# Kernel optimization log

Measured on AMD Instinct MI355X. Metric: run time of the kernel, lower is better.

The kernel has to match this reference:

```python
import jax, jax.numpy as jnp
import numpy as np

N_USERS = 20000
N_ITEMS = 30000
N = N_USERS + N_ITEMS          # total nodes
D = 64                          # embedding_dim
EXTRA = 1152                    # 768 metadata + 384 review
E = 500000                      # full-graph edges
NC = 100                        # clusters
HEADS = 2                       # per-layer GATConv heads
CG_HEADS = 4                    # GlobalGATOverClusters hard-codes heads=4
L = 2                           # num_layers
ED = 2                          # edge_dim


def _gat(x, ei, ea, lin, a_src, a_dst, lin_e, a_edge, bias, heads, nnodes):
    """PyG GATConv: add self loops (edge_attr fill='mean'), concat=False -> head mean."""
    C = a_src.shape[-1]
    loop = jnp.arange(nnodes)
    src = jnp.concatenate([ei[0], loop])
    dst = jnp.concatenate([ei[1], loop])
    ea_full = jnp.concatenate([ea, jnp.broadcast_to(ea.mean(0), (nnodes, ea.shape[1]))], 0)
    xh = (x @ lin).reshape(nnodes, heads, C)            # [N,H,C]
    asrc = (xh * a_src).sum(-1)                         # [N,H]
    adst = (xh * a_dst).sum(-1)
    eh = (ea_full @ lin_e).reshape(-1, heads, C)        # [Etot,H,C]
    ae = (eh * a_edge).sum(-1)                          # [Etot,H]
    al = jax.nn.leaky_relu(asrc[src] + adst[dst] + ae, 0.2)
    amax = jax.ops.segment_max(al, dst, num_segments=nnodes)
    ex = jnp.exp(al - amax[dst])
    s = jax.ops.segment_sum(ex, dst, num_segments=nnodes)
    w = ex / (s[dst] + 1e-16)
    out = jax.ops.segment_sum(xh[src] * w[..., None], dst, num_segments=nnodes)
    return out.mean(1) + bias


def _graph_norm(x, weight, bias, mean_scale, eps=1e-5):
    mean = x.mean(0)
    out = x - mean_scale * mean
    var = (out * out).mean(0)
    return weight * out * jax.lax.rsqrt(var + eps) + bias


def _forward(product_extra_features, user_emb, item_emb, fus_w1, fus_b1, fus_w2, fus_b2,
             full_edge_attr, gcn_w, gcn_b,
             cg_lin, cg_att_src, cg_att_dst, cg_lin_edge, cg_att_edge, cg_bias, cluster_edge_attr,
             gat_lin, gat_att_src, gat_att_dst, gat_lin_edge, gat_att_edge, gat_bias,
             gn_weight, gn_bias, gn_mean_scale,
             full_edge_index, cluster_assignment, cluster_edge_index):
    # fusion MLP on item side (dropout is identity at inference)
    h = jnp.maximum(jnp.concatenate([item_emb, product_extra_features], -1) @ fus_w1 + fus_b1, 0.0)
    enriched_items = h @ fus_w2 + fus_b2
    X = jnp.concatenate([user_emb, enriched_items], 0)  # [N, D]

    # per-cluster GCN == one GCN over intra-cluster edges + self loops;
    # nodes in clusters with zero intra edges keep original features
    ei0, ei1 = full_edge_index[0], full_edge_index[1]
    intra = cluster_assignment[ei0] == cluster_assignment[ei1]
    loop = jnp.arange(N)
    row = jnp.concatenate([ei0, loop])
    col = jnp.concatenate([ei1, loop])
    ew = jnp.concatenate([intra.astype(X.dtype), jnp.ones((N,), X.dtype)])
    deg = jax.ops.segment_sum(ew, col, num_segments=N)
    dinv = jnp.where(deg > 0, jax.lax.rsqrt(deg), 0.0)
    norm = dinv[row] * ew * dinv[col]
    xw = X @ gcn_w
    gcn_out = jax.ops.segment_sum(xw[row] * norm[:, None], col, num_segments=N) + gcn_b
    cl_has_edge = jax.ops.segment_sum(intra.astype(jnp.int32), cluster_assignment[ei0], num_segments=NC) > 0
    Xc = jnp.where(cl_has_edge[cluster_assignment][:, None], gcn_out, X)

    # mean pool per cluster
    cnt = jax.ops.segment_sum(jnp.ones((N,), X.dtype), cluster_assignment, num_segments=NC)
    pooled = jax.ops.segment_sum(Xc, cluster_assignment, num_segments=NC) / jnp.maximum(cnt, 1.0)[:, None]

    # global GAT over clusters (inter-cluster multigraph, precomputed)
    cl_upd = _gat(pooled, cluster_edge_index, cluster_edge_attr,
                  cg_lin, cg_att_src, cg_att_dst, cg_lin_edge, cg_att_edge, cg_bias, CG_HEADS, NC)
    Xcomb = Xc + cl_upd[cluster_assignment]

    # full-graph GAT stack with GraphNorm + residual ELU (dropout identity)
    for i in range(L):
        Xin = Xcomb
        g = _gat(Xcomb, full_edge_index, full_edge_attr,
                 gat_lin[i], gat_att_src[i], gat_att_dst[i],
                 gat_lin_edge[i], gat_att_edge[i], gat_bias[i], HEADS, N)
        g = _graph_norm(g, gn_weight[i], gn_bias[i], gn_mean_scale[i])
        Xcomb = jax.nn.elu(g + Xin)

    return Xcomb[:N_USERS], Xcomb[N_USERS:]


def setup_inputs() -> dict:
    rng = np.random.default_rng(0)
    fei = rng.integers(0, N, size=(2, E)).astype(np.int32)
    ca = rng.integers(0, NC, size=(N,)).astype(np.int32)
    fea = rng.random((E, ED)).astype(np.float32)
    # build_cluster_graph: one cluster edge per inter-cluster full edge
    cu, cv = ca[fei[0]], ca[fei[1]]
    m = cu != cv
    cei = np.stack([cu[m], cv[m]]).astype(np.int32)
    cea = fea[m]

    key = jax.random.key(0)
    ks = jax.random.split(key, 24)
    nrm = lambda k, shp, s=0.05: jax.random.normal(k, shp, dtype=jnp.float32) * s
    return {
        'product_extra_features': jax.random.normal(ks[0], (N_ITEMS, EXTRA), dtype=jnp.float32),
        'user_emb': nrm(ks[1], (N_USERS, D), 1.0),
        'item_emb': nrm(ks[2], (N_ITEMS, D), 1.0),
        'fus_w1': nrm(ks[3], (D + EXTRA, 2 * D)),
        'fus_b1': jnp.zeros((2 * D,), jnp.float32),
        'fus_w2': nrm(ks[4], (2 * D, D)),
        'fus_b2': jnp.zeros((D,), jnp.float32),
        'full_edge_attr': jnp.asarray(fea),
        'gcn_w': nrm(ks[5], (D, D)),
        'gcn_b': jnp.zeros((D,), jnp.float32),
        'cg_lin': nrm(ks[6], (D, CG_HEADS * D)),
        'cg_att_src': nrm(ks[7], (CG_HEADS, D)),
        'cg_att_dst': nrm(ks[8], (CG_HEADS, D)),
        'cg_lin_edge': nrm(ks[9], (ED, CG_HEADS * D)),
        'cg_att_edge': nrm(ks[10], (CG_HEADS, D)),
        'cg_bias': jnp.zeros((D,), jnp.float32),
        'cluster_edge_attr': jnp.asarray(cea),
        'gat_lin': nrm(ks[11], (L, D, HEADS * D)),
        'gat_att_src': nrm(ks[12], (L, HEADS, D)),
        'gat_att_dst': nrm(ks[13], (L, HEADS, D)),
        'gat_lin_edge': nrm(ks[14], (L, ED, HEADS * D)),
        'gat_att_edge': nrm(ks[15], (L, HEADS, D)),
        'gat_bias': jnp.zeros((L, D), jnp.float32),
        'gn_weight': jnp.ones((L, D), jnp.float32),
        'gn_bias': jnp.zeros((L, D), jnp.float32),
        'gn_mean_scale': jnp.ones((L, D), jnp.float32),
        'full_edge_index': jnp.asarray(fei),
        'cluster_assignment': jnp.asarray(ca),
        'cluster_edge_index': jnp.asarray(cei),
    }


def reference(product_extra_features, user_emb, item_emb, fus_w1, fus_b1, fus_w2, fus_b2,
              full_edge_attr, gcn_w, gcn_b,
              cg_lin, cg_att_src, cg_att_dst, cg_lin_edge, cg_att_edge, cg_bias, cluster_edge_attr,
              gat_lin, gat_att_src, gat_att_dst, gat_lin_edge, gat_att_edge, gat_bias,
              gn_weight, gn_bias, gn_mean_scale,
              full_edge_index, cluster_assignment, cluster_edge_index):
    return _forward(product_extra_features, user_emb, item_emb, fus_w1, fus_b1, fus_w2, fus_b2,
                    full_edge_attr, gcn_w, gcn_b,
                    cg_lin, cg_att_src, cg_att_dst, cg_lin_edge, cg_att_edge, cg_bias, cluster_edge_attr,
                    gat_lin, gat_att_src, gat_att_dst, gat_lin_edge, gat_att_edge, gat_bias,
                    gn_weight, gn_bias, gn_mean_scale,
                    full_edge_index, cluster_assignment, cluster_edge_index)
```

## Files before the change

kernel.cpp:

```cpp
#include <hip/hip_runtime.h>
#include <hip/hip_bf16.h>

#define N_USERS 20000
#define N_ITEMS 30000
#define NTOT    50000
#define DIM     64
#define EXTRA_D 1152
#define E_EDGES 500000
#define NC      100
#define KTOT    1216
#define KSTEPS  38
#define PPART   16

#define B_COPY 1250
#define B_W1   608
#define B_W2   32
#define B_CC   64
#define B_FEI  1954
#define B_CEI  256
#define PREP_GRID (B_COPY+B_W1+B_W2+B_CC+B_FEI+B_CEI)

#define FUS_BLKS ((N_ITEMS+127)/128)
#define SCAN1_BLKS ((NTOT+1023)/1024)
#define SC3_BLKS ((NTOT+255)/256)
#define FILL_BLKS ((E_EDGES+255)/256)
#define DEG_BLKS ((NTOT+3)/4)

typedef __attribute__((ext_vector_type(8))) short short8;
typedef __attribute__((ext_vector_type(4))) float v4f;

__device__ __forceinline__ float wred_sum(float v){
#pragma unroll
  for(int o=32;o;o>>=1) v += __shfl_xor(v,o,64);
  return v;
}
__device__ __forceinline__ int wred_sumi(int v){
#pragma unroll
  for(int o=32;o;o>>=1) v += __shfl_xor(v,o,64);
  return v;
}
__device__ __forceinline__ float lrelu(float x){ return x>0.f? x : 0.2f*x; }
__device__ __forceinline__ short f2bf(float f){
  unsigned u=__float_as_uint(f);
  unsigned r=(u + 0x7FFFu + ((u>>16)&1u))>>16;
  return (short)r;
}
__device__ __forceinline__ unsigned pack_bf2(float x, float y){
  return (unsigned)(unsigned short)f2bf(x) | ((unsigned)(unsigned short)f2bf(y)<<16);
}

__global__ __launch_bounds__(256) void prep_all_kernel(
    const float* __restrict__ u, float* __restrict__ X,
    const float* __restrict__ w1, short* __restrict__ w1t,
    const float* __restrict__ w2, short* __restrict__ w2t,
    const int* __restrict__ ca, int* __restrict__ ccnt,
    const int* __restrict__ fei, const float* __restrict__ fea,
    int* __restrict__ cnt_dst, int* __restrict__ clflag, int* __restrict__ degI,
    float2* __restrict__ partA,
    const int* __restrict__ cei, const float* __restrict__ cea, int Ec,
    int* __restrict__ ccnt_dst, float2* __restrict__ partB)
{
  __shared__ int hist[NC];
  __shared__ float2 w4[4];
  const int b=blockIdx.x, t=threadIdx.x;
  const int lane=t&63, wv=t>>6;
  if(b < B_COPY){
    int i = b*256+t;
    ((float4*)X)[i] = ((const float4*)u)[i];
  } else if(b < B_COPY+B_W1){
    int i = (b-B_COPY)*256+t;
    int row = i>>7, n = i&127;
    int s = row>>5, kk = row&31;
    w1t[s*4096 + n*32 + kk] = f2bf(w1[i]);
  } else if(b < B_COPY+B_W1+B_W2){
    int i = (b-B_COPY-B_W1)*256+t;
    int n = i>>6, c = i&63;
    w2t[c*128 + n] = f2bf(w2[i]);
  } else if(b < B_COPY+B_W1+B_W2+B_CC){
    int bb = b-(B_COPY+B_W1+B_W2);
    for(int i=t;i<NC;i+=256) hist[i]=0;
    __syncthreads();
    for(int n=bb*256+t; n<NTOT; n+=B_CC*256) atomicAdd(&hist[ca[n]],1);
    __syncthreads();
    for(int i=t;i<NC;i+=256) if(hist[i]) atomicAdd(&ccnt[i],hist[i]);
  } else if(b < B_COPY+B_W1+B_W2+B_CC+B_FEI){
    int bb = b-(B_COPY+B_W1+B_W2+B_CC);
    int e = bb*256+t;
    float a0=0.f,a1=0.f;
    if(e<E_EDGES){
      int s=fei[e], d=fei[E_EDGES+e];
      atomicAdd(&cnt_dst[d],1);
      int cs=ca[s];
      if(cs==ca[d]){ clflag[cs]=1; atomicAdd(&degI[d],1); }
      float2 v=*(const float2*)(fea+2*e);
      a0=v.x; a1=v.y;
    }
    a0=wred_sum(a0); a1=wred_sum(a1);
    if(lane==0) w4[wv]=make_float2(a0,a1);
    __syncthreads();
    if(t==0){ float2 r=w4[0]; for(int i=1;i<4;i++){r.x+=w4[i].x; r.y+=w4[i].y;} partA[bb]=r; }
  } else {
    int bb = b-(B_COPY+B_W1+B_W2+B_CC+B_FEI);
    for(int i=t;i<NC;i+=256) hist[i]=0;
    __syncthreads();
    float a0=0.f,a1=0.f;
    for(int e=bb*256+t; e<Ec; e+=B_CEI*256){
      atomicAdd(&hist[cei[Ec+e]],1);
      float2 v=*(const float2*)(cea+2*e);
      a0+=v.x; a1+=v.y;
    }
    a0=wred_sum(a0); a1=wred_sum(a1);
    if(lane==0) w4[wv]=make_float2(a0,a1);
    __syncthreads();
    if(t==0){ float2 r=w4[0]; for(int i=1;i<4;i++){r.x+=w4[i].x; r.y+=w4[i].y;} partB[bb]=r; }
    for(int i=t;i<NC;i+=256) if(hist[i]) atomicAdd(&ccnt_dst[i],hist[i]);
  }
}

__global__ __launch_bounds__(256) void fus_scan_kernel(
    const float* __restrict__ item, const float* __restrict__ extra,
    const short* __restrict__ w1t, const float* __restrict__ b1,
    const short* __restrict__ w2t, const float* __restrict__ b2,
    float* __restrict__ X,
    const float2* __restrict__ partA, const float2* __restrict__ partB, int Ec,
    const float* __restrict__ cg_le, const float* __restrict__ cg_ae,
    const float* __restrict__ gat_le, const float* __restrict__ gat_ae,
    float* __restrict__ coefs,
    const int* __restrict__ cnt_dst, int* __restrict__ incl, int* __restrict__ bsum)
{
  __shared__ short As[128*40];
  __shared__ short Bs[128*40];
  __shared__ short Hs[128*136];
  __shared__ int ssc[256];
  const int tid = threadIdx.x;
  const int b = blockIdx.x;
  if(b < FUS_BLKS){
    const int blk = b;
    const int w = tid>>6, lane = tid&63, quad = lane>>4, l16 = lane&15;
    const int mw = w&1, nw = w>>1;

    v4f acc[4][4];
#pragma unroll
    for(int a=0;a<4;a++)
#pragma unroll
      for(int c=0;c<4;c++) acc[a][c] = (v4f){0.f,0.f,0.f,0.f};

    const int arow = tid>>3;
    const int aoff = (tid&7)*4;
    for(int s=0;s<KSTEPS;s++){
      const int k0 = s*32;
#pragma unroll
      for(int it=0;it<4;it++){
        int r = arow + it*32;
        int col = k0 + aoff;
        int gr = blk*128 + r; if(gr >= N_ITEMS) gr = N_ITEMS-1;
        float4 v = (col < DIM) ? *(const float4*)(item + (size_t)gr*DIM + col)
                               : *(const float4*)(extra + (size_t)gr*EXTRA_D + (col-DIM));
        short4 bv; bv.x=f2bf(v.x); bv.y=f2bf(v.y); bv.z=f2bf(v.z); bv.w=f2bf(v.w);
        *(short4*)&As[r*40 + aoff] = bv;
      }
#pragma unroll
      for(int it=0;it<2;it++){
        int idx = tid + it*256;
        int4 v = *(const int4*)(w1t + (size_t)s*4096 + idx*8);
        int n = idx>>2, kk = (idx&3)*8;
        *(int4*)&Bs[n*40 + kk] = v;
      }
      __syncthreads();
      short8 af[4], bf_[4];
#pragma unroll
      for(int i=0;i<4;i++){
        int m = mw*64 + i*16 + l16;
        af[i]  = *(const short8*)&As[m*40 + quad*8];
        int n = nw*64 + i*16 + l16;
        bf_[i] = *(const short8*)&Bs[n*40 + quad*8];
      }
#pragma unroll
      for(int mi=0;mi<4;mi++)
#pragma unroll
        for(int ni=0;ni<4;ni++)
          acc[mi][ni] = __builtin_amdgcn_mfma_f32_16x16x32_bf16(af[mi], bf_[ni], acc[mi][ni], 0,0,0);
      __syncthreads();
    }

#pragma unroll
    for(int ni=0;ni<4;ni++){
      int n = nw*64 + ni*16 + l16;
      float bias = b1[n];
#pragma unroll
      for(int mi=0;mi<4;mi++){
        int mbase = mw*64 + mi*16 + quad*4;
#pragma unroll
        for(int r=0;r<4;r++){
          float hv = fmaxf(acc[mi][ni][r] + bias, 0.f);
          Hs[(mbase+r)*136 + n] = f2bf(hv);
        }
      }
    }
    __syncthreads();

    v4f acc2[2][4];
#pragma unroll
    for(int a=0;a<2;a++)
#pragma unroll
      for(int c=0;c<4;c++) acc2[a][c] = (v4f){0.f,0.f,0.f,0.f};
#pragma unroll
    for(int ks=0;ks<4;ks++){
      short8 ha[2];
#pragma unroll
      for(int mi=0;mi<2;mi++){
        int m = w*32 + mi*16 + l16;
        ha[mi] = *(const short8*)&Hs[m*136 + ks*32 + quad*8];
      }
#pragma unroll
      for(int ni=0;ni<4;ni++){
        int c = ni*16 + l16;
        short8 wb = *(const short8*)(w2t + c*128 + ks*32 + quad*8);
#pragma unroll
        for(int mi=0;mi<2;mi++)
          acc2[mi][ni] = __builtin_amdgcn_mfma_f32_16x16x32_bf16(ha[mi], wb, acc2[mi][ni], 0,0,0);
      }
    }
#pragma unroll
    for(int ni=0;ni<4;ni++){
      int c = ni*16 + l16;
      float b2v = b2[c];
#pragma unroll
      for(int mi=0;mi<2;mi++){
        int mbase = w*32 + mi*16 + quad*4;
#pragma unroll
        for(int r=0;r<4;r++){
          int row = blk*128 + mbase + r;
          if(row < N_ITEMS) X[(size_t)(N_USERS+row)*64 + c] = acc2[mi][ni][r] + b2v;
        }
      }
    }
  } else if(b == FUS_BLKS){
    int lane=tid&63; int wv=tid>>6;
    {
      int hh=wv;
      float v0 = cg_le[hh*64+lane]*cg_ae[hh*64+lane];
      float v1 = cg_le[256 + hh*64+lane]*cg_ae[hh*64+lane];
      v0=wred_sum(v0); v1=wred_sum(v1);
      if(lane==0){ coefs[8+hh]=v0; coefs[12+hh]=v1; }
    }
    {
      int l=wv>>1, hh=wv&1;
      float v0 = gat_le[l*256 + hh*64+lane]     * gat_ae[l*128+hh*64+lane];
      float v1 = gat_le[l*256 + 128 + hh*64+lane]* gat_ae[l*128+hh*64+lane];
      v0=wred_sum(v0); v1=wred_sum(v1);
      if(lane==0){ coefs[16+l*2+hh]=v0; coefs[20+l*2+hh]=v1; }
    }
    __syncthreads();
    if(wv==0){
      float sx=0.f, sy=0.f;
      for(int i=lane;i<B_FEI;i+=64){ float2 v=partA[i]; sx+=v.x; sy+=v.y; }
      sx=wred_sum(sx); sy=wred_sum(sy);
      if(lane==0){ coefs[4]=sx/(float)E_EDGES; coefs[5]=sy/(float)E_EDGES; }
    }
    if(wv==1){
      float sx=0.f, sy=0.f;
      for(int i=lane;i<B_CEI;i+=64){ float2 v=partB[i]; sx+=v.x; sy+=v.y; }
      sx=wred_sum(sx); sy=wred_sum(sy);
      if(lane==0){ coefs[6]=sx/(float)Ec; coefs[7]=sy/(float)Ec; }
    }
  } else {
    int sb = b-FUS_BLKS-1;
    int base = sb*1024 + tid*4;
    int a0=(base  <NTOT)?cnt_dst[base  ]+1:0;
    int a1=(base+1<NTOT)?cnt_dst[base+1]+1:0;
    int a2=(base+2<NTOT)?cnt_dst[base+2]+1:0;
    int a3=(base+3<NTOT)?cnt_dst[base+3]+1:0;
    int l1=a0+a1, l2=l1+a2, l3=l2+a3;
    ssc[tid]=l3; __syncthreads();
    for(int off=1;off<256;off<<=1){
      int v=(tid>=off)?ssc[tid-off]:0; __syncthreads();
      ssc[tid]+=v; __syncthreads();
    }
    int prev = tid? ssc[tid-1]:0;
    if(base  <NTOT) incl[base  ]=prev+a0;
    if(base+1<NTOT) incl[base+1]=prev+l1;
    if(base+2<NTOT) incl[base+2]=prev+l2;
    if(base+3<NTOT) incl[base+3]=prev+l3;
    if(tid==255) bsum[sb]=ssc[255];
  }
}

__global__ __launch_bounds__(256) void mid_kernel(
    const int* __restrict__ incl, const int* __restrict__ cnt,
    const int* __restrict__ bsum, int* __restrict__ offs, int* __restrict__ fillptr,
    const float* __restrict__ coefs, int2* __restrict__ slot2,
    const int* __restrict__ degI, float* __restrict__ dinv,
    const int* __restrict__ ccnt_dst, int* __restrict__ coffs, int* __restrict__ cfillp,
    const float* __restrict__ X, const float* __restrict__ gw, float* __restrict__ xw)
{
  __shared__ float Wl[64*64];
  __shared__ float rowb[4][64];
  __shared__ int sprev;
  const int b=blockIdx.x, t=threadIdx.x;
  if(b < SC3_BLKS){
    int blk10 = b>>2;
    if(t<64){
      int v = (t<blk10)? bsum[t] : 0;
      v = wred_sumi(v);
      if(t==0) sprev=v;
    }
    __syncthreads();
    unsigned pk = pack_bf2(coefs[4], coefs[5]);
    int i = b*256+t;
    if(i<NTOT){
      int c=cnt[i];
      int start = sprev + incl[i] - (c+1);
      offs[i]=start; fillptr[i]=start;
      slot2[start+c]=make_int2(i,(int)pk);
      dinv[i]=rsqrtf((float)(degI[i]+1));
    }
    if(i==0) offs[NTOT]=E_EDGES+NTOT;
  } else if(b == SC3_BLKS){
    if(t<64){
      int lane=t;
      int v0 = (2*lane<NC)? ccnt_dst[2*lane]:0;
      int v1 = (2*lane+1<NC)? ccnt_dst[2*lane+1]:0;
      int pair=v0+v1;
      int sc=pair;
#pragma unroll
      for(int o=1;o<64;o<<=1){ int t2=__shfl_up(sc,o,64); if(lane>=o) sc+=t2; }
      int excl = sc - pair;
      if(2*lane<NC){ coffs[2*lane]=excl; cfillp[2*lane]=excl; }
      if(2*lane+1<NC){ coffs[2*lane+1]=excl+v0; cfillp[2*lane+1]=excl+v0; }
      if(lane==63) coffs[NC]=sc;
    }
  } else {
    int bb=b-SC3_BLKS-1;
    const int lane=t&63, wv=t>>6;
    for(int i=t;i<4096;i+=256) Wl[i]=gw[i];
    __syncthreads();
    for(int r=bb*4+wv; r<NTOT; r+=1024*4){
      rowb[wv][lane]=X[(size_t)r*64+lane];
      float acc=0.f;
#pragma unroll 8
      for(int k=0;k<64;k++) acc+=rowb[wv][k]*Wl[k*64+lane];
      xw[(size_t)r*64+lane]=acc;
    }
  }
}

__global__ __launch_bounds__(256) void fill_kernel(
    const int* __restrict__ fei, const float* __restrict__ fea,
    int* __restrict__ fillptr, int2* __restrict__ slot2,
    const int* __restrict__ cei, const float* __restrict__ cea, int Ec,
    int* __restrict__ cfillp, int* __restrict__ cslot_src, float2* __restrict__ cslot_ea)
{
  __shared__ int hist[NC];
  __shared__ int base[NC];
  const int b=blockIdx.x, t=threadIdx.x;
  if(b<FILL_BLKS){
    int e=b*256+t;
    if(e<E_EDGES){
      int dst=fei[E_EDGES+e], src=fei[e];
      int pos=atomicAdd(&fillptr[dst],1);
      float2 v=*(const float2*)(fea+2*e);
      slot2[pos]=make_int2(src,(int)pack_bf2(v.x,v.y));
    }
  } else {
    int bb=b-FILL_BLKS;
    const int chunk=(Ec+127)/128;
    const int beg=bb*chunk;
    const int end=min(beg+chunk,Ec);
    for(int i=t;i<NC;i+=256) hist[i]=0;
    __syncthreads();
    for(int e=beg+t;e<end;e+=256) atomicAdd(&hist[cei[Ec+e]],1);
    __syncthreads();
    for(int i=t;i<NC;i+=256){
      int h=hist[i];
      base[i] = h ? atomicAdd(&cfillp[i],h) : 0;
      hist[i]=0;
    }
    __syncthreads();
    for(int e=beg+t;e<end;e+=256){
      int d=cei[Ec+e];
      int pos = base[d] + atomicAdd(&hist[d],1);
      cslot_src[pos]=cei[e];
      cslot_ea[pos]=make_float2(cea[2*e],cea[2*e+1]);
    }
  }
}

__global__ __launch_bounds__(256) void gcn_agg_kernel(const float* __restrict__ X,
    const float* __restrict__ xw, const float* __restrict__ gcn_b,
    const int* __restrict__ offs, const int2* __restrict__ slot2, const int* __restrict__ ca,
    const float* __restrict__ dinv, const int* __restrict__ flag,
    float* __restrict__ Xc, float* __restrict__ psum){
  __shared__ float2 stg[4][64];
  int lane=threadIdx.x&63, wv=threadIdx.x>>6;
  int n=blockIdx.x*4+wv; if(n>=NTOT) return;
  int beg=offs[n], end=offs[n+1], myca=ca[n];
  float acc=0.f;
  for(int c0=beg;c0<end;c0+=64){
    int j=c0+lane;
    float coef=0.f; int s=0;
    if(j<end){
      s=slot2[j].x;
      if(ca[s]==myca) coef=dinv[s];
    }
    stg[wv][lane]=make_float2(__int_as_float(s),coef);
    unsigned long long bal=__ballot(coef!=0.f);
    while(bal){
      int k=__builtin_ctzll(bal); bal&=bal-1;
      float2 sc=stg[wv][k];
      acc += sc.y * xw[(size_t)__float_as_int(sc.x)*64+lane];
    }
  }
  float gout = dinv[n]*acc + gcn_b[lane];
  float xc = flag[myca] ? gout : X[(size_t)n*64+lane];
  Xc[(size_t)n*64+lane]=xc;
  atomicAdd(&psum[(size_t)(blockIdx.x&(PPART-1))*NC*64 + myca*64+lane], xc);
}

__global__ __launch_bounds__(256) void cluster_prep_kernel(const float* __restrict__ psum,
    const int* __restrict__ ccnt, const float* __restrict__ cg_lin,
    const float* __restrict__ as_, const float* __restrict__ ad_,
    float* __restrict__ xh_c, float* __restrict__ asrc_c, float* __restrict__ adst_c){
  __shared__ float prow[64];
  const int c=blockIdx.x, t=threadIdx.x;
  if(t<64){
    float a=0.f;
#pragma unroll
    for(int p=0;p<PPART;p++) a += psum[(size_t)p*NC*64 + c*64 + t];
    prow[t]=a/fmaxf((float)ccnt[c],1.f);
  }
  __syncthreads();
  float acc=0.f;
#pragma unroll 8
  for(int k=0;k<64;k++) acc += prow[k]*cg_lin[k*256+t];
  xh_c[c*256+t]=acc;
  int lane=t&63, hh=t>>6;
  float s=wred_sum(acc*as_[hh*64+lane]);
  float d=wred_sum(acc*ad_[hh*64+lane]);
  if(lane==0){ asrc_c[c*4+hh]=s; adst_c[c*4+hh]=d; }
}
__global__ __launch_bounds__(256) void cluster_agg_kernel(
    const int* __restrict__ coffs, const int* __restrict__ cslot_src, const float2* __restrict__ cslot_ea,
    const float* __restrict__ asrc_c, const float* __restrict__ adst_c, const float* __restrict__ coefs,
    const float* __restrict__ xh_c, const float* __restrict__ cg_bias, float* __restrict__ cl_upd)
{
  __shared__ float sas[NC*4];
  __shared__ float sW[NC*4];
  __shared__ float ssum[4];
  __shared__ float red[4][64];
  const int c=blockIdx.x, t=threadIdx.x;
  for(int i=t;i<NC*4;i+=256){ sas[i]=asrc_c[i]; sW[i]=0.f; }
  __syncthreads();
  float ad[4], A0[4], A1[4];
#pragma unroll
  for(int h=0;h<4;h++){ ad[h]=adst_c[c*4+h]; A0[h]=coefs[8+h]; A1[h]=coefs[12+h]; }
  const int beg=coffs[c], end=coffs[c+1];
  for(int j=beg+t;j<end;j+=256){
    int s=cslot_src[j]; float2 e=cslot_ea[j];
#pragma unroll
    for(int h=0;h<4;h++){
      float al=lrelu(sas[s*4+h]+ad[h]+e.x*A0[h]+e.y*A1[h]);
      atomicAdd(&sW[s*4+h], __expf(al));
    }
  }
  if(t<4){
    float al=lrelu(sas[c*4+t]+ad[t]+coefs[6]*A0[t]+coefs[7]*A1[t]);
    atomicAdd(&sW[c*4+t], __expf(al));
  }
  __syncthreads();
  const int h=t>>6, lane=t&63;
  float p=0.f;
  if(lane<NC)    p += sW[lane*4+h];
  if(lane+64<NC) p += sW[(lane+64)*4+h];
  p=wred_sum(p);
  if(lane==0) ssum[h]=p+1e-16f;
  __syncthreads();
  float inv=1.f/ssum[h];
  float acc=0.f;
  for(int s=0;s<NC;s++) acc += sW[s*4+h]*xh_c[s*256+h*64+lane];
  red[h][lane]=acc*inv;
  __syncthreads();
  if(t<64) cl_upd[c*64+t]=0.25f*(red[0][t]+red[1][t]+red[2][t]+red[3][t])+cg_bias[t];
}

__global__ __launch_bounds__(256) void gat_xh0_kernel(const float* __restrict__ Xc,
    const float* __restrict__ cl_upd, const int* __restrict__ ca,
    const float* __restrict__ lin, const float* __restrict__ att_s, const float* __restrict__ att_d,
    float2* __restrict__ xh2, float* __restrict__ asrc, float* __restrict__ adst,
    float* __restrict__ Xa){
  __shared__ __align__(16) float Wl[64*128];
  __shared__ float rowb[4][64];
  int t=threadIdx.x;
  for(int i=t;i<8192;i+=256) Wl[i]=lin[i];
  __syncthreads();
  int lane=t&63, wv=t>>6;
  float as0=att_s[lane], as1=att_s[64+lane], ad0=att_d[lane], ad1=att_d[64+lane];
  for(int r=blockIdx.x*4+wv; r<NTOT; r+=gridDim.x*4){
    float xv = Xc[(size_t)r*64+lane] + cl_upd[ca[r]*64+lane];
    Xa[(size_t)r*64+lane]=xv;
    rowb[wv][lane]=xv;
    float x0=0.f,x1=0.f;
#pragma unroll 8
    for(int k=0;k<64;k++){ float q=rowb[wv][k]; x0+=q*Wl[k*128+lane]; x1+=q*Wl[k*128+64+lane]; }
    xh2[(size_t)r*64+lane]=make_float2(x0,x1);
    float p0=wred_sum(x0*as0);
    float p1=wred_sum(x1*as1);
    float q0=wred_sum(x0*ad0);
    float q1=wred_sum(x1*ad1);
    if(lane==0){ asrc[2*r]=p0; asrc[2*r+1]=p1; adst[2*r]=q0; adst[2*r+1]=q1; }
  }
}
__global__ __launch_bounds__(256) void gat_xh1_kernel(const float* __restrict__ g,
    const float* __restrict__ Xres, const float* __restrict__ stats,
    const float* __restrict__ gnw, const float* __restrict__ gnb, const float* __restrict__ gnms,
    const float* __restrict__ lin, const float* __restrict__ att_s, const float* __restrict__ att_d,
    float2* __restrict__ xh2, float* __restrict__ asrc, float* __restrict__ adst,
    float* __restrict__ Xb){
  __shared__ __align__(16) float Wl[64*128];
  __shared__ float rowb[4][64];
  int t=threadIdx.x;
  for(int i=t;i<8192;i+=256) Wl[i]=lin[i];
  __syncthreads();
  int lane=t&63, wv=t>>6;
  const float invN = 1.f/(float)NTOT;
  float m=stats[lane]*invN;
  float mm=gnms[lane]*m;
  float gwv=rsqrtf(stats[64+lane]*invN - 2.f*mm*m + mm*mm + 1e-5f)*gnw[lane];
  float gbv=gnb[lane];
  float as0=att_s[lane], as1=att_s[64+lane], ad0=att_d[lane], ad1=att_d[64+lane];
  for(int r=blockIdx.x*4+wv; r<NTOT; r+=gridDim.x*4){
    float z=(g[(size_t)r*64+lane]-mm)*gwv+gbv + Xres[(size_t)r*64+lane];
    float xv = z>0.f? z : __expf(z)-1.f;
    Xb[(size_t)r*64+lane]=xv;
    rowb[wv][lane]=xv;
    float x0=0.f,x1=0.f;
#pragma unroll 8
    for(int k=0;k<64;k++){ float q=rowb[wv][k]; x0+=q*Wl[k*128+lane]; x1+=q*Wl[k*128+64+lane]; }
    xh2[(size_t)r*64+lane]=make_float2(x0,x1);
    float p0=wred_sum(x0*as0);
    float p1=wred_sum(x1*as1);
    float q0=wred_sum(x0*ad0);
    float q1=wred_sum(x1*ad1);
    if(lane==0){ asrc[2*r]=p0; asrc[2*r+1]=p1; adst[2*r]=q0; adst[2*r+1]=q1; }
  }
}

__global__ __launch_bounds__(256) void gat_agg_kernel(const float2* __restrict__ xh2,
    const float2* __restrict__ asrc, const float2* __restrict__ adst,
    const int* __restrict__ offs, const int2* __restrict__ slot2,
    const float* __restrict__ coefs, int layer, const float* __restrict__ bias,
    float* __restrict__ g){
  __shared__ float4 stg[4][64];
  int lane=threadIdx.x&63, wv=threadIdx.x>>6;
  int n=blockIdx.x*4+wv; if(n>=NTOT) return;
  float A00=coefs[16+layer*2+0], A01=coefs[16+layer*2+1];
  float A10=coefs[20+layer*2+0], A11=coefs[20+layer*2+1];
  int beg=offs[n], end=offs[n+1];
  float2 adn=adst[n];
  float s0=0.f,s1=0.f,acc0=0.f,acc1=0.f;
  for(int c0=beg;c0<end;c0+=64){
    int j=c0+lane;
    float ex0=0.f,ex1=0.f; int s=0;
    if(j<end){
      int2 sl=slot2[j];
      s=sl.x;
      unsigned p=(unsigned)sl.y;
      float e0=__uint_as_float(p<<16);
      float e1=__uint_as_float(p&0xffff0000u);
      float2 a=asrc[s];
      ex0=__expf(lrelu(a.x+adn.x+e0*A00+e1*A10));
      ex1=__expf(lrelu(a.y+adn.y+e0*A01+e1*A11));
    }
    s0+=ex0; s1+=ex1;
    stg[wv][lane]=make_float4(__int_as_float(s),ex0,ex1,0.f);
    int cnt=min(64,end-c0);
    int k=0;
    for(; k+4<=cnt; k+=4){
      float4 w0=stg[wv][k], w1=stg[wv][k+1], w2=stg[wv][k+2], w3=stg[wv][k+3];
      float2 x0=xh2[(size_t)__float_as_int(w0.x)*64+lane];
      float2 x1=xh2[(size_t)__float_as_int(w1.x)*64+lane];
      float2 x2=xh2[(size_t)__float_as_int(w2.x)*64+lane];
      float2 x3=xh2[(size_t)__float_as_int(w3.x)*64+lane];
      acc0 += w0.y*x0.x + w1.y*x1.x + w2.y*x2.x + w3.y*x3.x;
      acc1 += w0.z*x0.y + w1.z*x1.y + w2.z*x2.y + w3.z*x3.y;
    }
    for(; k<cnt; k++){
      float4 ws=stg[wv][k];
      float2 xv=xh2[(size_t)__float_as_int(ws.x)*64+lane];
      acc0 += ws.y*xv.x;
      acc1 += ws.z*xv.y;
    }
  }
  s0=wred_sum(s0); s1=wred_sum(s1);
  g[(size_t)n*64+lane]=0.5f*(acc0/(s0+1e-16f)+acc1/(s1+1e-16f))+bias[lane];
}
__global__ __launch_bounds__(256) void stats_kernel(const float* __restrict__ g,
    float* __restrict__ stats){
  __shared__ float s1[64], s2[64];
  int t=threadIdx.x;
  if(t<64){s1[t]=0.f;s2[t]=0.f;}
  __syncthreads();
  float a0=0.f,a1=0.f,a2=0.f,a3=0.f,b0=0.f,b1=0.f,b2=0.f,b3=0.f;
  int i0=blockIdx.x*256+t;
  for(int i=i0;i<NTOT*16;i+=gridDim.x*256){
    float4 v=((const float4*)g)[i];
    a0+=v.x;a1+=v.y;a2+=v.z;a3+=v.w;
    b0+=v.x*v.x;b1+=v.y*v.y;b2+=v.z*v.z;b3+=v.w*v.w;
  }
  int d0=(i0&15)*4;
  atomicAdd(&s1[d0],a0); atomicAdd(&s1[d0+1],a1); atomicAdd(&s1[d0+2],a2); atomicAdd(&s1[d0+3],a3);
  atomicAdd(&s2[d0],b0); atomicAdd(&s2[d0+1],b1); atomicAdd(&s2[d0+2],b2); atomicAdd(&s2[d0+3],b3);
  __syncthreads();
  if(t<64) atomicAdd(&stats[t],s1[t]);
  else if(t<128) atomicAdd(&stats[t],s2[t-64]);
}
__global__ __launch_bounds__(256) void gnorm_elu_kernel(const float* __restrict__ g,
    const float* __restrict__ Xin, const float* __restrict__ stats,
    const float* __restrict__ gw, const float* __restrict__ gb, const float* __restrict__ gms,
    float* __restrict__ outp){
  const float invN = 1.f/(float)NTOT;
  int i0=blockIdx.x*256+threadIdx.x;
  int d0=(i0&15)*4;
  float mmv[4],gwv[4],gbv[4];
#pragma unroll
  for(int j=0;j<4;j++){
    int d=d0+j;
    float m=stats[d]*invN;
    float mm=gms[d]*m;
    mmv[j]=mm;
    gwv[j]=rsqrtf(stats[64+d]*invN-2.f*mm*m+mm*mm+1e-5f)*gw[d];
    gbv[j]=gb[d];
  }
  for(int i=i0;i<NTOT*16;i+=gridDim.x*256){
    float4 gv=((const float4*)g)[i];
    float4 xv=((const float4*)Xin)[i];
    float4 o; float z;
    z=(gv.x-mmv[0])*gwv[0]+gbv[0]+xv.x; o.x = z>0.f? z : __expf(z)-1.f;
    z=(gv.y-mmv[1])*gwv[1]+gbv[1]+xv.y; o.y = z>0.f? z : __expf(z)-1.f;
    z=(gv.z-mmv[2])*gwv[2]+gbv[2]+xv.z; o.z = z>0.f? z : __expf(z)-1.f;
    z=(gv.w-mmv[3])*gwv[3]+gbv[3]+xv.w; o.w = z>0.f? z : __expf(z)-1.f;
    ((float4*)outp)[i]=o;
  }
}

extern "C" void kernel_launch(void* const* d_in, const int* in_sizes, int n_in,
                              void* d_out, int out_size, void* d_ws, size_t ws_size,
                              hipStream_t stream)
{
  const float* extra = (const float*)d_in[0];
  const float* user  = (const float*)d_in[1];
  const float* item  = (const float*)d_in[2];
  const float* fw1 = (const float*)d_in[3];
  const float* fb1 = (const float*)d_in[4];
  const float* fw2 = (const float*)d_in[5];
  const float* fb2 = (const float*)d_in[6];
  const float* fea = (const float*)d_in[7];
  const float* gcn_w = (const float*)d_in[8];
  const float* gcn_b = (const float*)d_in[9];
  const float* cg_lin = (const float*)d_in[10];
  const float* cg_as = (const float*)d_in[11];
  const float* cg_ad = (const float*)d_in[12];
  const float* cg_le = (const float*)d_in[13];
  const float* cg_ae = (const float*)d_in[14];
  const float* cg_bias = (const float*)d_in[15];
  const float* cea = (const float*)d_in[16];
  const float* gat_lin = (const float*)d_in[17];
  const float* gat_as = (const float*)d_in[18];
  const float* gat_ad = (const float*)d_in[19];
  const float* gat_le = (const float*)d_in[20];
  const float* gat_ae = (const float*)d_in[21];
  const float* gat_bias = (const float*)d_in[22];
  const float* gn_w = (const float*)d_in[23];
  const float* gn_b = (const float*)d_in[24];
  const float* gn_ms = (const float*)d_in[25];
  const int* fei = (const int*)d_in[26];
  const int* ca  = (const int*)d_in[27];
  const int* cei = (const int*)d_in[28];
  const int Ec = in_sizes[16]/2;
  float* outp = (float*)d_out;

  char* w = (char*)d_ws;
  auto alloc=[&](size_t b)->char*{ char* p=w; w += (b+255)&~(size_t)255; return p; };

  char* z0 = w;
  int* cnt_dst = (int*)alloc((size_t)NTOT*4);
  int* degI = (int*)alloc((size_t)NTOT*4);
  int* clflag = (int*)alloc(NC*4);
  int* ccnt = (int*)alloc(NC*4);
  int* ccnt_dst = (int*)alloc(NC*4);
  float* psum = (float*)alloc((size_t)PPART*NC*64*4);
  float* stats0 = (float*)alloc(128*4);
  float* stats1 = (float*)alloc(128*4);
  size_t zbytes = (size_t)(w - z0);

  float2* partA = (float2*)alloc(2048*8);
  float2* partB = (float2*)alloc(256*8);
  float* coefs = (float*)alloc(32*4);
  int* offs = (int*)alloc((size_t)(NTOT+1)*4);
  int* incl = (int*)alloc((size_t)NTOT*4);
  int* bsum = (int*)alloc(64*4);
  int* fillptr = (int*)alloc((size_t)NTOT*4);
  int2* slot2 = (int2*)alloc((size_t)(E_EDGES+NTOT)*8);
  int* coffs = (int*)alloc((size_t)(NC+1)*4);
  int* cfillp = (int*)alloc((size_t)NC*4);
  int* cslot_src = (int*)alloc((size_t)E_EDGES*4);
  float2* cslot_ea = (float2*)alloc((size_t)E_EDGES*8);
  float* dinv = (float*)alloc((size_t)NTOT*4);
  float* xh_c = (float*)alloc(NC*256*4);
  float* asrc_c = (float*)alloc(NC*4*4);
  float* adst_c = (float*)alloc(NC*4*4);
  float* cl_upd = (float*)alloc(NC*64*4);
  float* asrc = (float*)alloc((size_t)NTOT*2*4);
  float* adst = (float*)alloc((size_t)NTOT*2*4);
  short* w1t = (short*)alloc((size_t)KSTEPS*4096*2);
  short* w2t = (short*)alloc((size_t)64*128*2);
  float* bufA = (float*)alloc((size_t)NTOT*64*4);
  float* bufB = (float*)alloc((size_t)NTOT*64*4);
  float* bufC = (float*)alloc((size_t)NTOT*64*4);
  float* bufD = (float*)alloc((size_t)NTOT*64*4);
  float* bufE = (float*)alloc((size_t)NTOT*128*4);

  float* X  = bufA; float* g  = bufA;
  float* Xc = bufB;
  float* xw = bufC; float* Xb = bufC;
  float* Xa = bufD;
  float2* xh2 = (float2*)bufE;

  hipMemsetAsync(z0, 0, zbytes, stream);

  prep_all_kernel<<<PREP_GRID,256,0,stream>>>(user, X, fw1, w1t, fw2, w2t, ca, ccnt,
                                              fei, fea, cnt_dst, clflag, degI, partA,
                                              cei, cea, Ec, ccnt_dst, partB);
  fus_scan_kernel<<<FUS_BLKS+1+SCAN1_BLKS,256,0,stream>>>(item, extra, w1t, fb1, w2t, fb2, X,
                                              partA, partB, Ec, cg_le, cg_ae, gat_le, gat_ae, coefs,
                                              cnt_dst, incl, bsum);
  mid_kernel<<<SC3_BLKS+1+1024,256,0,stream>>>(incl, cnt_dst, bsum, offs, fillptr, coefs, slot2,
                                              degI, dinv, ccnt_dst, coffs, cfillp,
                                              X, gcn_w, xw);
  fill_kernel<<<FILL_BLKS+128,256,0,stream>>>(fei, fea, fillptr, slot2,
                                              cei, cea, Ec, cfillp, cslot_src, cslot_ea);

  gcn_agg_kernel<<<DEG_BLKS,256,0,stream>>>(X, xw, gcn_b, offs, slot2, ca, dinv, clflag, Xc, psum);
  cluster_prep_kernel<<<NC,256,0,stream>>>(psum, ccnt, cg_lin, cg_as, cg_ad, xh_c, asrc_c, adst_c);
  cluster_agg_kernel<<<NC,256,0,stream>>>(coffs, cslot_src, cslot_ea, asrc_c, adst_c, coefs,
                                          xh_c, cg_bias, cl_upd);

  gat_xh0_kernel<<<1024,256,0,stream>>>(Xc, cl_upd, ca, gat_lin, gat_as, gat_ad,
                                        xh2, asrc, adst, Xa);
  gat_agg_kernel<<<DEG_BLKS,256,0,stream>>>(xh2, (const float2*)asrc, (const float2*)adst,
                                            offs, slot2, coefs, 0, gat_bias, g);
  stats_kernel<<<128,256,0,stream>>>(g, stats0);
  gat_xh1_kernel<<<1024,256,0,stream>>>(g, Xa, stats0, gn_w, gn_b, gn_ms,
                                        gat_lin+64*128, gat_as+128, gat_ad+128,
                                        xh2, asrc, adst, Xb);
  gat_agg_kernel<<<DEG_BLKS,256,0,stream>>>(xh2, (const float2*)asrc, (const float2*)adst,
                                            offs, slot2, coefs, 1, gat_bias+64, g);
  stats_kernel<<<128,256,0,stream>>>(g, stats1);
  gnorm_elu_kernel<<<512,256,0,stream>>>(g, Xb, stats1, gn_w+64, gn_b+64, gn_ms+64, outp);
}
```

Before: 671.6 us.

## Fuse stats into GAT aggregation, merge cluster kernels, rebalance prep work

Fuses the column-sum and sum-of-squares GraphNorm statistics into the GAT aggregation kernel, which removes two stats kernels and a re-read of g. The two cluster kernels are merged into one, using reassociated algebra (attention projections through cg_lin, then aggregating pooled features before the linear map) so the xh_c intermediate is dropped. The user-embedding copy and cluster-count histogram move from the prep kernel into the fusion/scan launch to balance work across kernels. In exchange, there are per-block shared atomics in the hot aggregation kernel and more global atomics on the stats arrays, and each cluster block recomputes all cluster source scores.

After: 1.225 ms. 82.4% more time.

```diff
diff --git a/kernel.cpp b/kernel.cpp
--- a/kernel.cpp
+++ b/kernel.cpp
@@ -12,16 +12,18 @@
 #define KSTEPS  38
 #define PPART   16
 
-#define B_COPY 1250
+#define B_FEI  1954
 #define B_W1   608
 #define B_W2   32
-#define B_CC   64
-#define B_FEI  1954
 #define B_CEI  256
-#define PREP_GRID (B_COPY+B_W1+B_W2+B_CC+B_FEI+B_CEI)
+#define PREP_GRID (B_FEI+B_W1+B_W2+B_CEI)
 
 #define FUS_BLKS ((N_ITEMS+127)/128)
 #define SCAN1_BLKS ((NTOT+1023)/1024)
+#define B_COPY 1250
+#define B_CC   64
+#define FUS_GRID (FUS_BLKS+SCAN1_BLKS+1+B_COPY+B_CC)
+
 #define SC3_BLKS ((NTOT+255)/256)
 #define FILL_BLKS ((E_EDGES+255)/256)
 #define DEG_BLKS ((NTOT+3)/4)
@@ -49,11 +51,10 @@
   return (unsigned)(unsigned short)f2bf(x) | ((unsigned)(unsigned short)f2bf(y)<<16);
 }
 
-__global__ __launch_bounds__(256) void prep_all_kernel(
-    const float* __restrict__ u, float* __restrict__ X,
+__global__ __launch_bounds__(256) void prep_edges_kernel(
     const float* __restrict__ w1, short* __restrict__ w1t,
     const float* __restrict__ w2, short* __restrict__ w2t,
-    const int* __restrict__ ca, int* __restrict__ ccnt,
+    const int* __restrict__ ca,
     const int* __restrict__ fei, const float* __restrict__ fea,
     int* __restrict__ cnt_dst, int* __restrict__ clflag, int* __restrict__ degI,
     float2* __restrict__ partA,
@@ -64,28 +65,8 @@
   __shared__ float2 w4[4];
   const int b=blockIdx.x, t=threadIdx.x;
   const int lane=t&63, wv=t>>6;
-  if(b < B_COPY){
-    int i = b*256+t;
-    ((float4*)X)[i] = ((const float4*)u)[i];
-  } else if(b < B_COPY+B_W1){
-    int i = (b-B_COPY)*256+t;
-    int row = i>>7, n = i&127;
-    int s = row>>5, kk = row&31;
-    w1t[s*4096 + n*32 + kk] = f2bf(w1[i]);
-  } else if(b < B_COPY+B_W1+B_W2){
-    int i = (b-B_COPY-B_W1)*256+t;
-    int n = i>>6, c = i&63;
-    w2t[c*128 + n] = f2bf(w2[i]);
-  } else if(b < B_COPY+B_W1+B_W2+B_CC){
-    int bb = b-(B_COPY+B_W1+B_W2);
-    for(int i=t;i<NC;i+=256) hist[i]=0;
-    __syncthreads();
-    for(int n=bb*256+t; n<NTOT; n+=B_CC*256) atomicAdd(&hist[ca[n]],1);
-    __syncthreads();
-    for(int i=t;i<NC;i+=256) if(hist[i]) atomicAdd(&ccnt[i],hist[i]);
-  } else if(b < B_COPY+B_W1+B_W2+B_CC+B_FEI){
-    int bb = b-(B_COPY+B_W1+B_W2+B_CC);
-    int e = bb*256+t;
+  if(b < B_FEI){
+    int e = b*256+t;
     float a0=0.f,a1=0.f;
     if(e<E_EDGES){
       int s=fei[e], d=fei[E_EDGES+e];
@@ -98,9 +79,18 @@
     a0=wred_sum(a0); a1=wred_sum(a1);
     if(lane==0) w4[wv]=make_float2(a0,a1);
     __syncthreads();
-    if(t==0){ float2 r=w4[0]; for(int i=1;i<4;i++){r.x+=w4[i].x; r.y+=w4[i].y;} partA[bb]=r; }
+    if(t==0){ float2 r=w4[0]; for(int i=1;i<4;i++){r.x+=w4[i].x; r.y+=w4[i].y;} partA[b]=r; }
+  } else if(b < B_FEI+B_W1){
+    int i = (b-B_FEI)*256+t;
+    int row = i>>7, n = i&127;
+    int s = row>>5, kk = row&31;
+    w1t[s*4096 + n*32 + kk] = f2bf(w1[i]);
+  } else if(b < B_FEI+B_W1+B_W2){
+    int i = (b-B_FEI-B_W1)*256+t;
+    int n = i>>6, c = i&63;
+    w2t[c*128 + n] = f2bf(w2[i]);
   } else {
-    int bb = b-(B_COPY+B_W1+B_W2+B_CC+B_FEI);
+    int bb = b-(B_FEI+B_W1+B_W2);
     for(int i=t;i<NC;i+=256) hist[i]=0;
     __syncthreads();
     float a0=0.f,a1=0.f;
@@ -126,7 +116,8 @@
     const float* __restrict__ cg_le, const float* __restrict__ cg_ae,
     const float* __restrict__ gat_le, const float* __restrict__ gat_ae,
     float* __restrict__ coefs,
-    const int* __restrict__ cnt_dst, int* __restrict__ incl, int* __restrict__ bsum)
+    const int* __restrict__ cnt_dst, int* __restrict__ incl, int* __restrict__ bsum,
+    const float* __restrict__ u, const int* __restrict__ ca, int* __restrict__ ccnt)
 {
   __shared__ short As[128*40];
   __shared__ short Bs[128*40];
@@ -235,37 +226,8 @@
         }
       }
     }
-  } else if(b == FUS_BLKS){
-    int lane=tid&63; int wv=tid>>6;
-    {
-      int hh=wv;
-      float v0 = cg_le[hh*64+lane]*cg_ae[hh*64+lane];
-      float v1 = cg_le[256 + hh*64+lane]*cg_ae[hh*64+lane];
-      v0=wred_sum(v0); v1=wred_sum(v1);
-      if(lane==0){ coefs[8+hh]=v0; coefs[12+hh]=v1; }
-    }
-    {
-      int l=wv>>1, hh=wv&1;
-      float v0 = gat_le[l*256 + hh*64+lane]     * gat_ae[l*128+hh*64+lane];
-      float v1 = gat_le[l*256 + 128 + hh*64+lane]* gat_ae[l*128+hh*64+lane];
-      v0=wred_sum(v0); v1=wred_sum(v1);
-      if(lane==0){ coefs[16+l*2+hh]=v0; coefs[20+l*2+hh]=v1; }
-    }
-    __syncthreads();
-    if(wv==0){
-      float sx=0.f, sy=0.f;
-      for(int i=lane;i<B_FEI;i+=64){ float2 v=partA[i]; sx+=v.x; sy+=v.y; }
-      sx=wred_sum(sx); sy=wred_sum(sy);
-      if(lane==0){ coefs[4]=sx/(float)E_EDGES; coefs[5]=sy/(float)E_EDGES; }
-    }
-    if(wv==1){
-      float sx=0.f, sy=0.f;
-      for(int i=lane;i<B_CEI;i+=64){ float2 v=partB[i]; sx+=v.x; sy+=v.y; }
-      sx=wred_sum(sx); sy=wred_sum(sy);
-      if(lane==0){ coefs[6]=sx/(float)Ec; coefs[7]=sy/(float)Ec; }
-    }
-  } else {
-    int sb = b-FUS_BLKS-1;
+  } else if(b < FUS_BLKS+SCAN1_BLKS){
+    int sb = b-FUS_BLKS;
     int base = sb*1024 + tid*4;
     int a0=(base  <NTOT)?cnt_dst[base  ]+1:0;
     int a1=(base+1<NTOT)?cnt_dst[base+1]+1:0;
@@ -283,6 +245,46 @@
     if(base+2<NTOT) incl[base+2]=prev+l2;
     if(base+3<NTOT) incl[base+3]=prev+l3;
     if(tid==255) bsum[sb]=ssc[255];
+  } else if(b == FUS_BLKS+SCAN1_BLKS){
+    int lane=tid&63; int wv=tid>>6;
+    {
+      int hh=wv;
+      float v0 = cg_le[hh*64+lane]*cg_ae[hh*64+lane];
+      float v1 = cg_le[256 + hh*64+lane]*cg_ae[hh*64+lane];
+      v0=wred_sum(v0); v1=wred_sum(v1);
+      if(lane==0){ coefs[8+hh]=v0; coefs[12+hh]=v1; }
+    }
+    {
+      int l=wv>>1, hh=wv&1;
+      float v0 = gat_le[l*256 + hh*64+lane]     * gat_ae[l*128+hh*64+lane];
+      float v1 = gat_le[l*256 + 128 + hh*64+lane]* gat_ae[l*128+hh*64+lane];
+      v0=wred_sum(v0); v1=wred_sum(v1);
+      if(lane==0){ coefs[16+l*2+hh]=v0; coefs[20+l*2+hh]=v1; }
+    }
+    __syncthreads();
+    if(wv==0){
+      float sx=0.f, sy=0.f;
+      for(int i=lane;i<B_FEI;i+=64){ float2 v=partA[i]; sx+=v.x; sy+=v.y; }
+      sx=wred_sum(sx); sy=wred_sum(sy);
+      if(lane==0){ coefs[4]=sx/(float)E_EDGES; coefs[5]=sy/(float)E_EDGES; }
+    }
+    if(wv==1){
+      float sx=0.f, sy=0.f;
+      for(int i=lane;i<B_CEI;i+=64){ float2 v=partB[i]; sx+=v.x; sy+=v.y; }
+      sx=wred_sum(sx); sy=wred_sum(sy);
+      if(lane==0){ coefs[6]=sx/(float)Ec; coefs[7]=sy/(float)Ec; }
+    }
+  } else if(b < FUS_BLKS+SCAN1_BLKS+1+B_COPY){
+    int i = (b-FUS_BLKS-SCAN1_BLKS-1)*256+tid;
+    ((float4*)X)[i] = ((const float4*)u)[i];
+  } else {
+    __shared__ int hist2[NC];
+    int bb = b-(FUS_BLKS+SCAN1_BLKS+1+B_COPY);
+    for(int i=tid;i<NC;i+=256) hist2[i]=0;
+    __syncthreads();
+    for(int n=bb*256+tid; n<NTOT; n+=B_CC*256) atomicAdd(&hist2[ca[n]],1);
+    __syncthreads();
+    for(int i=tid;i<NC;i+=256) if(hist2[i]) atomicAdd(&ccnt[i],hist2[i]);
   }
 }
 
@@ -393,7 +395,7 @@
     float* __restrict__ Xc, float* __restrict__ psum){
   __shared__ float2 stg[4][64];
   int lane=threadIdx.x&63, wv=threadIdx.x>>6;
-  int n=blockIdx.x*4+wv; if(n>=NTOT) return;
+  int n=blockIdx.x*4+wv;
   int beg=offs[n], end=offs[n+1], myca=ca[n];
   float acc=0.f;
   for(int c0=beg;c0<end;c0+=64){
@@ -417,68 +419,90 @@
   atomicAdd(&psum[(size_t)(blockIdx.x&(PPART-1))*NC*64 + myca*64+lane], xc);
 }
 
-__global__ __launch_bounds__(256) void cluster_prep_kernel(const float* __restrict__ psum,
-    const int* __restrict__ ccnt, const float* __restrict__ cg_lin,
-    const float* __restrict__ as_, const float* __restrict__ ad_,
-    float* __restrict__ xh_c, float* __restrict__ asrc_c, float* __restrict__ adst_c){
-  __shared__ float prow[64];
-  const int c=blockIdx.x, t=threadIdx.x;
-  if(t<64){
-    float a=0.f;
-#pragma unroll
-    for(int p=0;p<PPART;p++) a += psum[(size_t)p*NC*64 + c*64 + t];
-    prow[t]=a/fmaxf((float)ccnt[c],1.f);
-  }
-  __syncthreads();
-  float acc=0.f;
-#pragma unroll 8
-  for(int k=0;k<64;k++) acc += prow[k]*cg_lin[k*256+t];
-  xh_c[c*256+t]=acc;
-  int lane=t&63, hh=t>>6;
-  float s=wred_sum(acc*as_[hh*64+lane]);
-  float d=wred_sum(acc*ad_[hh*64+lane]);
-  if(lane==0){ asrc_c[c*4+hh]=s; adst_c[c*4+hh]=d; }
-}
-__global__ __launch_bounds__(256) void cluster_agg_kernel(
+__global__ __launch_bounds__(256) void cluster_all_kernel(
+    const float* __restrict__ psum, const int* __restrict__ ccnt,
+    const float* __restrict__ cg_lin, const float* __restrict__ as_, const float* __restrict__ ad_,
     const int* __restrict__ coffs, const int* __restrict__ cslot_src, const float2* __restrict__ cslot_ea,
-    const float* __restrict__ asrc_c, const float* __restrict__ adst_c, const float* __restrict__ coefs,
-    const float* __restrict__ xh_c, const float* __restrict__ cg_bias, float* __restrict__ cl_upd)
+    const float* __restrict__ coefs, const float* __restrict__ cg_bias, float* __restrict__ cl_upd)
 {
+  __shared__ float pool[NC*64];
   __shared__ float sas[NC*4];
+  __shared__ float sad[4];
   __shared__ float sW[NC*4];
+  __shared__ float Ps[4][64], Pd[4][64];
+  __shared__ float qq[4][64];
   __shared__ float ssum[4];
   __shared__ float red[4][64];
   const int c=blockIdx.x, t=threadIdx.x;
-  for(int i=t;i<NC*4;i+=256){ sas[i]=asrc_c[i]; sW[i]=0.f; }
-  __syncthreads();
-  float ad[4], A0[4], A1[4];
-#pragma unroll
-  for(int h=0;h<4;h++){ ad[h]=adst_c[c*4+h]; A0[h]=coefs[8+h]; A1[h]=coefs[12+h]; }
+  const int lane=t&63, hh=t>>6;
+  for(int i=t;i<NC*64;i+=256){
+    float a=0.f;
+#pragma unroll
+    for(int p=0;p<PPART;p++) a += psum[(size_t)p*NC*64 + i];
+    pool[i]=a/fmaxf((float)ccnt[i>>6],1.f);
+  }
+  {
+    float av=as_[hh*64+lane], dv=ad_[hh*64+lane];
+    for(int k=0;k<64;k++){
+      float cl=cg_lin[k*256+hh*64+lane];
+      float s=wred_sum(cl*av);
+      float d=wred_sum(cl*dv);
+      if(lane==0){ Ps[hh][k]=s; Pd[hh][k]=d; }
+    }
+  }
+  for(int i=t;i<NC*4;i+=256) sW[i]=0.f;
+  __syncthreads();
+  for(int i=t;i<NC*4;i+=256){
+    int s=i>>2, h=i&3;
+    float a=0.f;
+#pragma unroll 8
+    for(int k=0;k<64;k++) a += pool[s*64+k]*Ps[h][k];
+    sas[i]=a;
+  }
+  if(t<4){
+    float a=0.f;
+#pragma unroll 8
+    for(int k=0;k<64;k++) a += pool[c*64+k]*Pd[t][k];
+    sad[t]=a;
+  }
+  __syncthreads();
+  float ad4[4], A0[4], A1[4];
+#pragma unroll
+  for(int h=0;h<4;h++){ ad4[h]=sad[h]; A0[h]=coefs[8+h]; A1[h]=coefs[12+h]; }
   const int beg=coffs[c], end=coffs[c+1];
   for(int j=beg+t;j<end;j+=256){
     int s=cslot_src[j]; float2 e=cslot_ea[j];
 #pragma unroll
     for(int h=0;h<4;h++){
-      float al=lrelu(sas[s*4+h]+ad[h]+e.x*A0[h]+e.y*A1[h]);
+      float al=lrelu(sas[s*4+h]+ad4[h]+e.x*A0[h]+e.y*A1[h]);
       atomicAdd(&sW[s*4+h], __expf(al));
     }
   }
   if(t<4){
-    float al=lrelu(sas[c*4+t]+ad[t]+coefs[6]*A0[t]+coefs[7]*A1[t]);
+    float al=lrelu(sas[c*4+t]+ad4[t]+coefs[6]*A0[t]+coefs[7]*A1[t]);
     atomicAdd(&sW[c*4+t], __expf(al));
   }
   __syncthreads();
-  const int h=t>>6, lane=t&63;
-  float p=0.f;
-  if(lane<NC)    p += sW[lane*4+h];
-  if(lane+64<NC) p += sW[(lane+64)*4+h];
-  p=wred_sum(p);
-  if(lane==0) ssum[h]=p+1e-16f;
-  __syncthreads();
-  float inv=1.f/ssum[h];
-  float acc=0.f;
-  for(int s=0;s<NC;s++) acc += sW[s*4+h]*xh_c[s*256+h*64+lane];
-  red[h][lane]=acc*inv;
+  {
+    float p=0.f;
+    if(lane<NC)    p += sW[lane*4+hh];
+    if(lane+64<NC) p += sW[(lane+64)*4+hh];
+    p=wred_sum(p);
+    if(lane==0) ssum[hh]=p+1e-16f;
+  }
+  {
+    float a=0.f;
+    for(int s=0;s<NC;s++) a += sW[s*4+hh]*pool[s*64+lane];
+    qq[hh][lane]=a;
+  }
+  __syncthreads();
+  {
+    float inv=1.f/ssum[hh];
+    float a=0.f;
+#pragma unroll 4
+    for(int k=0;k<64;k++) a += qq[hh][k]*cg_lin[k*256+hh*64+lane];
+    red[hh][lane]=a*inv;
+  }
   __syncthreads();
   if(t<64) cl_upd[c*64+t]=0.25f*(red[0][t]+red[1][t]+red[2][t]+red[3][t])+cg_bias[t];
 }
@@ -549,15 +573,19 @@
     const float2* __restrict__ asrc, const float2* __restrict__ adst,
     const int* __restrict__ offs, const int2* __restrict__ slot2,
     const float* __restrict__ coefs, int layer, const float* __restrict__ bias,
-    float* __restrict__ g){
+    float* __restrict__ g, float* __restrict__ stats){
   __shared__ float4 stg[4][64];
-  int lane=threadIdx.x&63, wv=threadIdx.x>>6;
-  int n=blockIdx.x*4+wv; if(n>=NTOT) return;
+  __shared__ float s1[64], s2[64];
+  int t=threadIdx.x;
+  int lane=t&63, wv=t>>6;
+  if(t<64){ s1[t]=0.f; s2[t]=0.f; }
+  __syncthreads();
+  int n=blockIdx.x*4+wv;
   float A00=coefs[16+layer*2+0], A01=coefs[16+layer*2+1];
   float A10=coefs[20+layer*2+0], A11=coefs[20+layer*2+1];
   int beg=offs[n], end=offs[n+1];
   float2 adn=adst[n];
-  float s0=0.f,s1=0.f,acc0=0.f,acc1=0.f;
+  float s0=0.f,sB=0.f,acc0=0.f,acc1=0.f;
   for(int c0=beg;c0<end;c0+=64){
     int j=c0+lane;
     float ex0=0.f,ex1=0.f; int s=0;
@@ -571,7 +599,7 @@
       ex0=__expf(lrelu(a.x+adn.x+e0*A00+e1*A10));
       ex1=__expf(lrelu(a.y+adn.y+e0*A01+e1*A11));
     }
-    s0+=ex0; s1+=ex1;
+    s0+=ex0; sB+=ex1;
     stg[wv][lane]=make_float4(__int_as_float(s),ex0,ex1,0.f);
     int cnt=min(64,end-c0);
     int k=0;
@@ -591,29 +619,16 @@
       acc1 += ws.z*xv.y;
     }
   }
-  s0=wred_sum(s0); s1=wred_sum(s1);
-  g[(size_t)n*64+lane]=0.5f*(acc0/(s0+1e-16f)+acc1/(s1+1e-16f))+bias[lane];
-}
-__global__ __launch_bounds__(256) void stats_kernel(const float* __restrict__ g,
-    float* __restrict__ stats){
-  __shared__ float s1[64], s2[64];
-  int t=threadIdx.x;
-  if(t<64){s1[t]=0.f;s2[t]=0.f;}
-  __syncthreads();
-  float a0=0.f,a1=0.f,a2=0.f,a3=0.f,b0=0.f,b1=0.f,b2=0.f,b3=0.f;
-  int i0=blockIdx.x*256+t;
-  for(int i=i0;i<NTOT*16;i+=gridDim.x*256){
-    float4 v=((const float4*)g)[i];
-    a0+=v.x;a1+=v.y;a2+=v.z;a3+=v.w;
-    b0+=v.x*v.x;b1+=v.y*v.y;b2+=v.z*v.z;b3+=v.w*v.w;
-  }
-  int d0=(i0&15)*4;
-  atomicAdd(&s1[d0],a0); atomicAdd(&s1[d0+1],a1); atomicAdd(&s1[d0+2],a2); atomicAdd(&s1[d0+3],a3);
-  atomicAdd(&s2[d0],b0); atomicAdd(&s2[d0+1],b1); atomicAdd(&s2[d0+2],b2); atomicAdd(&s2[d0+3],b3);
+  s0=wred_sum(s0); sB=wred_sum(sB);
+  float gv = 0.5f*(acc0/(s0+1e-16f)+acc1/(sB+1e-16f))+bias[lane];
+  g[(size_t)n*64+lane]=gv;
+  atomicAdd(&s1[lane],gv);
+  atomicAdd(&s2[lane],gv*gv);
   __syncthreads();
   if(t<64) atomicAdd(&stats[t],s1[t]);
   else if(t<128) atomicAdd(&stats[t],s2[t-64]);
 }
+
 __global__ __launch_bounds__(256) void gnorm_elu_kernel(const float* __restrict__ g,
     const float* __restrict__ Xin, const float* __restrict__ stats,
     const float* __restrict__ gw, const float* __restrict__ gb, const float* __restrict__ gms,
@@ -706,9 +721,6 @@
   int* cslot_src = (int*)alloc((size_t)E_EDGES*4);
   float2* cslot_ea = (float2*)alloc((size_t)E_EDGES*8);
   float* dinv = (float*)alloc((size_t)NTOT*4);
-  float* xh_c = (float*)alloc(NC*256*4);
-  float* asrc_c = (float*)alloc(NC*4*4);
-  float* adst_c = (float*)alloc(NC*4*4);
   float* cl_upd = (float*)alloc(NC*64*4);
   float* asrc = (float*)alloc((size_t)NTOT*2*4);
   float* adst = (float*)alloc((size_t)NTOT*2*4);
@@ -728,12 +740,12 @@
 
   hipMemsetAsync(z0, 0, zbytes, stream);
 
-  prep_all_kernel<<<PREP_GRID,256,0,stream>>>(user, X, fw1, w1t, fw2, w2t, ca, ccnt,
+  prep_edges_kernel<<<PREP_GRID,256,0,stream>>>(fw1, w1t, fw2, w2t, ca,
                                               fei, fea, cnt_dst, clflag, degI, partA,
                                               cei, cea, Ec, ccnt_dst, partB);
-  fus_scan_kernel<<<FUS_BLKS+1+SCAN1_BLKS,256,0,stream>>>(item, extra, w1t, fb1, w2t, fb2, X,
+  fus_scan_kernel<<<FUS_GRID,256,0,stream>>>(item, extra, w1t, fb1, w2t, fb2, X,
                                               partA, partB, Ec, cg_le, cg_ae, gat_le, gat_ae, coefs,
-                                              cnt_dst, incl, bsum);
+                                              cnt_dst, incl, bsum, user, ca, ccnt);
   mid_kernel<<<SC3_BLKS+1+1024,256,0,stream>>>(incl, cnt_dst, bsum, offs, fillptr, coefs, slot2,
                                               degI, dinv, ccnt_dst, coffs, cfillp,
                                               X, gcn_w, xw);
@@ -741,20 +753,17 @@
                                               cei, cea, Ec, cfillp, cslot_src, cslot_ea);
 
   gcn_agg_kernel<<<DEG_BLKS,256,0,stream>>>(X, xw, gcn_b, offs, slot2, ca, dinv, clflag, Xc, psum);
-  cluster_prep_kernel<<<NC,256,0,stream>>>(psum, ccnt, cg_lin, cg_as, cg_ad, xh_c, asrc_c, adst_c);
-  cluster_agg_kernel<<<NC,256,0,stream>>>(coffs, cslot_src, cslot_ea, asrc_c, adst_c, coefs,
-                                          xh_c, cg_bias, cl_upd);
+  cluster_all_kernel<<<NC,256,0,stream>>>(psum, ccnt, cg_lin, cg_as, cg_ad,
+                                          coffs, cslot_src, cslot_ea, coefs, cg_bias, cl_upd);
 
   gat_xh0_kernel<<<1024,256,0,stream>>>(Xc, cl_upd, ca, gat_lin, gat_as, gat_ad,
                                         xh2, asrc, adst, Xa);
   gat_agg_kernel<<<DEG_BLKS,256,0,stream>>>(xh2, (const float2*)asrc, (const float2*)adst,
-                                            offs, slot2, coefs, 0, gat_bias, g);
-  stats_kernel<<<128,256,0,stream>>>(g, stats0);
+                                            offs, slot2, coefs, 0, gat_bias, g, stats0);
   gat_xh1_kernel<<<1024,256,0,stream>>>(g, Xa, stats0, gn_w, gn_b, gn_ms,
                                         gat_lin+64*128, gat_as+128, gat_ad+128,
                                         xh2, asrc, adst, Xb);
   gat_agg_kernel<<<DEG_BLKS,256,0,stream>>>(xh2, (const float2*)asrc, (const float2*)adst,
-                                            offs, slot2, coefs, 1, gat_bias+64, g);
-  stats_kernel<<<128,256,0,stream>>>(g, stats1);
+                                            offs, slot2, coefs, 1, gat_bias+64, g, stats1);
   gnorm_elu_kernel<<<512,256,0,stream>>>(g, Xb, stats1, gn_w+64, gn_b+64, gn_ms+64, outp);
 }
```
